# Performance work log

Hardware: AMD Instinct MI355X
Metric: run time of the kernel (lower is better)

Reference implementation:

```python
import jax, jax.numpy as jnp
import numpy as np

B, IN, T, E, S, K, W, HD = 4096, 512, 10, 16, 2, 4, 1024, 64


def setup_inputs() -> dict:
    key = jax.random.key(0)
    ks = jax.random.split(key, 12)
    he = lambda k, shp, fan: jax.random.normal(k, shp, jnp.float32) * (2.0 / fan) ** 0.5
    x = jax.random.normal(ks[0], (B, IN + T), jnp.float32)
    return {
        'x': x,
        'gk': he(ks[1], (T, E), T),
        'rk0': he(ks[2], (E, IN, W), IN),
        'rb0': jax.random.normal(ks[3], (E, W), jnp.float32) * 0.01,
        'rk1': he(ks[4], (E, W, W), W),
        'rb1': jax.random.normal(ks[5], (E, W), jnp.float32) * 0.01,
        'sk0': he(ks[6], (S, IN, W), IN),
        'sb0': jax.random.normal(ks[7], (S, W), jnp.float32) * 0.01,
        'sk1': he(ks[8], (S, W, W), W),
        'sb1': jax.random.normal(ks[9], (S, W), jnp.float32) * 0.01,
        'hk': he(ks[10], (T, W, HD), W),
        'hb': jax.random.normal(ks[11], (T, HD), jnp.float32) * 0.01,
    }


def reference(x, gk, rk0, rb0, rk1, rb1, sk0, sb0, sk1, sb1, hk, hb):
    task_idx = x[:, -T:]            # (B, T) task one-hot / features
    feat = x[:, :-T]                # (B, IN)

    # --- top-k routing on task features ---
    gating_logits = task_idx @ gk                       # (B, E)
    topk_idx = jnp.argsort(-gating_logits, axis=-1)[:, :K]  # (B, K)
    topk_logits = jnp.take_along_axis(gating_logits, topk_idx, axis=-1)
    topk_weights = jax.nn.softmax(topk_logits, axis=-1)     # (B, K)

    # --- routed experts: run every expert chain densely, gather at the end ---
    # h: (B, E, d); each expert's independent MLP chain over the same input.
    h = jnp.broadcast_to(feat[:, None, :], (B, E, IN))
    h = jax.nn.relu(jnp.einsum('bei,eij->bej', h, rk0) + rb0[None])  # (B, E, W)
    h = jax.nn.relu(jnp.einsum('bei,eij->bej', h, rk1) + rb1[None])  # (B, E, W)
    h_sel = jnp.take_along_axis(h, topk_idx[:, :, None], axis=1)     # (B, K, W)
    routed = jnp.einsum('bkw,bk->bw', h_sel, topk_weights)           # (B, W)

    # --- shared experts: all run, mean-combined ---
    hs = jnp.broadcast_to(feat[:, None, :], (B, S, IN))
    hs = jax.nn.relu(jnp.einsum('bsi,sij->bsj', hs, sk0) + sb0[None])
    hs = jax.nn.relu(jnp.einsum('bsi,sij->bsj', hs, sk1) + sb1[None])
    shared = hs.mean(axis=1)                                         # (B, W)

    features_out = jnp.tanh(routed + shared)                         # (B, W)

    # --- per-task heads, select by task id ---
    heads_out = jnp.einsum('bw,twd->btd', features_out, hk) + hb[None]  # (B, T, HD)
    task_indices = task_idx.argmax(axis=-1)                             # (B,)
    out = jnp.take_along_axis(heads_out, task_indices[:, None, None], axis=1)[:, 0]
    return out
```

## Files before the change

kernel.cpp:

```cpp
#include <hip/hip_runtime.h>

typedef unsigned short u16;
typedef __attribute__((ext_vector_type(8))) short bf16x8;
typedef __attribute__((ext_vector_type(4))) float f32x4;

constexpr int B_ = 4096, IN_ = 512, T_ = 10, E_ = 16, S_ = 2, K_ = 4, W_ = 1024, HD_ = 64;
constexpr int XROW = IN_ + T_;
constexpr int NPAIR = B_ * (K_ + S_);
constexpr int MTU = 208;
constexpr int GEMM_GRID = MTU * 8;
constexpr int GB_ = 16;
constexpr int CB_GRID = 1034;


#define GLL16(g, l) __builtin_amdgcn_global_load_lds( \
    (const __attribute__((address_space(1))) void*)(g), \
    (__attribute__((address_space(3))) void*)(l), 16, 0, 0)

__device__ __forceinline__ u16 f2bf(float x) {
    unsigned u = __float_as_uint(x);
    return (u16)((u + 0x7fffu + ((u >> 16) & 1u)) >> 16);
}
__device__ __forceinline__ float bf2f(u16 b) { return __uint_as_float(((unsigned)b) << 16); }

__global__ __launch_bounds__(256) void featconv(const float* __restrict__ x, u16* __restrict__ featb) {
    int i = blockIdx.x * 256 + threadIdx.x;
    int b = i >> 8;
    int c2 = (i & 255) * 2;
    float2 v = *(const float2*)(x + (size_t)b * XROW + c2);
    ushort2 o;
    o.x = f2bf(v.x);
    o.y = f2bf(v.y);
    *(ushort2*)(featb + (size_t)b * IN_ + c2) = o;
}

__global__ __launch_bounds__(256) void gate_kernel(const float* __restrict__ x, const float* __restrict__ gk,
                                                   int* __restrict__ top4p, float* __restrict__ w6,
                                                   int* __restrict__ task_id, int* __restrict__ tpp,
                                                   int* __restrict__ bct_e, int* __restrict__ bct_t) {
    __shared__ float sgk[T_ * E_];
    __shared__ int hist[E_];
    __shared__ int thist[T_];
    int blk = blockIdx.x, tid = threadIdx.x;
    int b = blk * 256 + tid;
    if (tid < T_ * E_) sgk[tid] = gk[tid];
    if (tid < E_) hist[tid] = 0;
    if (tid < T_) thist[tid] = 0;
    __syncthreads();
    float tv[T_];
#pragma unroll
    for (int i = 0; i < T_; ++i) tv[i] = x[(size_t)b * XROW + IN_ + i];
    float lg[E_];
#pragma unroll
    for (int e = 0; e < E_; ++e) {
        float s = 0.f;
#pragma unroll
        for (int i = 0; i < T_; ++i) s += tv[i] * sgk[i * E_ + e];
        lg[e] = s;
    }
    int idx[K_]; float val[K_];
#pragma unroll
    for (int k = 0; k < K_; ++k) {
        int bi = 0; float bv = -1e30f;
#pragma unroll
        for (int e = 0; e < E_; ++e)
            if (lg[e] > bv) { bv = lg[e]; bi = e; }
        idx[k] = bi; val[k] = bv; lg[bi] = -1e30f;
    }
    float m = val[0];
    float ex[K_]; float s = 0.f;
#pragma unroll
    for (int k = 0; k < K_; ++k) { ex[k] = expf(val[k] - m); s += ex[k]; }
    float inv = 1.f / s;
#pragma unroll
    for (int k = 0; k < K_; ++k) {
        int lp = atomicAdd(&hist[idx[k]], 1);
        top4p[b * K_ + k] = idx[k] | (lp << 8);
        w6[b * 6 + k] = ex[k] * inv;
    }
    w6[b * 6 + 4] = 0.5f;
    w6[b * 6 + 5] = 0.5f;
    int ti = 0; float tb = tv[0];
#pragma unroll
    for (int i = 1; i < T_; ++i)
        if (tv[i] > tb) { tb = tv[i]; ti = i; }
    task_id[b] = ti;
    tpp[b] = atomicAdd(&thist[ti], 1);
    __syncthreads();
    if (tid < E_) bct_e[blk * E_ + tid] = hist[tid];
    if (tid < T_) bct_t[blk * T_ + tid] = thist[tid];
}

__global__ void build_tables(const int* __restrict__ bct_e, const int* __restrict__ bct_t,
                             int* __restrict__ meta, int* __restrict__ blockbase,
                             int* __restrict__ tblockbase) {
    if (threadIdx.x != 0) return;
    int counts[E_];
    for (int e = 0; e < E_; ++e) {
        int s = 0;
        for (int blk = 0; blk < GB_; ++blk) s += bct_e[blk * E_ + e];
        counts[e] = s;
        meta[e] = s;
    }
    int a = 0;
    for (int e = 0; e < E_; ++e) { meta[16 + e] = a; a += counts[e]; }
    for (int e = 0; e < E_; ++e) {
        int run = meta[16 + e];
        for (int blk = 0; blk < GB_; ++blk) { blockbase[blk * E_ + e] = run; run += bct_e[blk * E_ + e]; }
    }
    int t = 0;
    for (int g = 0; g < 18; ++g) { meta[48 + g] = t; int c = (g < 16) ? counts[g] : B_; t += (c + 127) >> 7; }
    meta[66] = t;
    int tcnt[T_];
    for (int i = 0; i < T_; ++i) {
        int s = 0;
        for (int blk = 0; blk < GB_; ++blk) s += bct_t[blk * T_ + i];
        tcnt[i] = s;
        meta[91 + i] = s;
    }
    int pr = 0, br = 0;
    for (int i = 0; i < T_; ++i) {
        meta[70 + i] = pr;
        meta[80 + i] = br;
        pr += ((tcnt[i] + 3) >> 2) << 2;
        br += (tcnt[i] + 3) >> 2;
    }
    meta[90] = br;
    for (int i = 0; i < T_; ++i) {
        int run = meta[70 + i];
        for (int blk = 0; blk < GB_; ++blk) { tblockbase[blk * T_ + i] = run; run += bct_t[blk * T_ + i]; }
    }
}

__global__ __launch_bounds__(256) void scatter_kernel(const int* __restrict__ top4p,
                                                      const int* __restrict__ blockbase,
                                                      const int* __restrict__ task_id, const int* __restrict__ tpp,
                                                      const int* __restrict__ tblockbase,
                                                      int* __restrict__ pair_sample, int* __restrict__ pair_dst,
                                                      int* __restrict__ torder) {
    int blk = blockIdx.x, tid = threadIdx.x;
    int b = blk * 256 + tid;
#pragma unroll
    for (int k = 0; k < K_; ++k) {
        int v = top4p[b * K_ + k];
        int e = v & 0xFF, lp = v >> 8;
        int p = blockbase[blk * E_ + e] + lp;
        pair_sample[p] = b;
        pair_dst[p] = b * 6 + k;
    }
    pair_sample[B_ * K_ + b] = b;       pair_dst[B_ * K_ + b] = b * 6 + 4;
    pair_sample[B_ * K_ + B_ + b] = b;  pair_dst[B_ * K_ + B_ + b] = b * 6 + 5;
    torder[tblockbase[blk * T_ + task_id[b]] + tpp[b]] = b;
}

__global__ __launch_bounds__(256) void convbf16(const float* __restrict__ in, u16* __restrict__ out) {
    int i = blockIdx.x * 256 + threadIdx.x;
    float4 v = ((const float4*)in)[i];
    ushort4 o;
    o.x = f2bf(v.x); o.y = f2bf(v.y); o.z = f2bf(v.z); o.w = f2bf(v.w);
    ((ushort4*)out)[i] = o;
}

__global__ __launch_bounds__(256) void transconv2(const float* __restrict__ srcA, const float* __restrict__ srcB,
                                                  int splitZ, u16* __restrict__ out, int K, int N) {
    __shared__ float tile[32][33];
    int z = blockIdx.z;
    const float* src = (z < splitZ) ? (srcA + (size_t)z * K * N) : (srcB + (size_t)(z - splitZ) * K * N);
    int k0 = blockIdx.y * 32, n0 = blockIdx.x * 32;
    int tid = threadIdx.x;
    int r = tid >> 3, c4 = (tid & 7) * 4;
    float4 v = *(const float4*)(src + (size_t)(k0 + r) * N + n0 + c4);
    tile[r][c4 + 0] = v.x; tile[r][c4 + 1] = v.y; tile[r][c4 + 2] = v.z; tile[r][c4 + 3] = v.w;
    __syncthreads();
    ushort4 ov;
    ov.x = f2bf(tile[c4 + 0][r]);
    ov.y = f2bf(tile[c4 + 1][r]);
    ov.z = f2bf(tile[c4 + 2][r]);
    ov.w = f2bf(tile[c4 + 3][r]);
    *(ushort4*)(out + (size_t)z * N * K + (size_t)(n0 + r) * K + k0 + c4) = ov;
}

template <int K, int LAYER>
__global__ __launch_bounds__(256, 2) void gemm3(const u16* __restrict__ Asrc, const u16* __restrict__ wT,
                                                const float* __restrict__ rbias, const float* __restrict__ sbias,
                                                const int* __restrict__ pair_sample, const int* __restrict__ pair_dst,
                                                const int* __restrict__ meta, u16* __restrict__ outp) {
    __shared__ char lds[65536];
    const int* tpre = meta + 48;
    const int nwg = tpre[18] * 8;
    int p = blockIdx.x;
    if (p >= nwg) return;
    int q = nwg >> 3, r8 = nwg & 7;
    int xcd = p & 7, iofs = p >> 3;
    int lid = (xcd < r8 ? xcd * (q + 1) : r8 * (q + 1) + (xcd - r8) * q) + iofs;
    int mtu = lid >> 3, nt = lid & 7;
    int e = 0;
    while (mtu >= tpre[e + 1]) ++e;
    int mt = mtu - tpre[e];
    int off, cnt;
    if (e < E_) { off = meta[16 + e]; cnt = meta[e]; }
    else        { off = B_ * K_ + (e - E_) * B_; cnt = B_; }

    const int tid = threadIdx.x;
    const int srow = tid >> 3, sc = tid & 7;
    const u16* wTe = wT + (size_t)e * W_ * K;
    const u16* ab[4];
    const u16* bb[4];
#pragma unroll
    for (int r = 0; r < 4; ++r) {
        int row = r * 32 + srow;
        int swz = (sc ^ (row & 7)) * 8;
        int gm = mt * 128 + row;
        if (gm >= cnt) gm = cnt - 1;
        int arow = (LAYER == 1) ? pair_sample[off + gm] : (off + gm);
        ab[r] = Asrc + (size_t)arow * K + swz;
        bb[r] = wTe + (size_t)(nt * 128 + row) * K + swz;
    }

    auto STAGE = [&](int kt, int buf) {
        char* base = lds + buf * 32768;
#pragma unroll
        for (int r = 0; r < 4; ++r) GLL16(ab[r] + kt * 64, base + r * 4096 + tid * 16);
#pragma unroll
        for (int r = 0; r < 4; ++r) GLL16(bb[r] + kt * 64, base + 16384 + r * 4096 + tid * 16);
    };

    f32x4 acc[4][4];
#pragma unroll
    for (int i = 0; i < 4; ++i)
#pragma unroll
        for (int j = 0; j < 4; ++j) acc[i][j] = (f32x4){0.f, 0.f, 0.f, 0.f};

    const int lane = tid & 63, wid = tid >> 6;
    const int wr = wid >> 1, wc = wid & 1;
    const int fr = lane & 15;
    const int fkb = (lane >> 4) * 16;

    constexpr int NKT = K / 64;
    STAGE(0, 0);
    for (int kt = 0; kt < NKT; ++kt) {
        int cur = kt & 1;
        if (kt + 1 < NKT) {
            STAGE(kt + 1, cur ^ 1);
            asm volatile("s_waitcnt vmcnt(8)" ::: "memory");
        } else {
            asm volatile("s_waitcnt vmcnt(0)" ::: "memory");
        }
        __builtin_amdgcn_s_barrier();
        asm volatile("" ::: "memory");
        char* A = lds + cur * 32768;
        char* Bv = A + 16384;
#pragma unroll
        for (int kk = 0; kk < 2; ++kk) {
            bf16x8 af[4], bf[4];
#pragma unroll
            for (int i = 0; i < 4; ++i) {
                int arow = wr * 64 + i * 16 + fr;
                af[i] = *(const bf16x8*)(A + arow * 128 + ((kk * 64 + fkb) ^ ((arow & 7) << 4)));
                int brow = wc * 64 + i * 16 + fr;
                bf[i] = *(const bf16x8*)(Bv + brow * 128 + ((kk * 64 + fkb) ^ ((brow & 7) << 4)));
            }
            __builtin_amdgcn_s_setprio(1);
#pragma unroll
            for (int i = 0; i < 4; ++i)
#pragma unroll
                for (int j = 0; j < 4; ++j)
                    acc[i][j] = __builtin_amdgcn_mfma_f32_16x16x32_bf16(af[i], bf[j], acc[i][j], 0, 0, 0);
            __builtin_amdgcn_s_setprio(0);
        }
        asm volatile("" ::: "memory");
        __builtin_amdgcn_s_barrier();
    }

    __syncthreads();
    const float* bias = (e < E_) ? (rbias + (size_t)e * W_) : (sbias + (size_t)(e - E_) * W_);
#pragma unroll
    for (int i = 0; i < 4; ++i) {
#pragma unroll
        for (int reg = 0; reg < 4; ++reg) {
            int r = wr * 64 + i * 16 + (lane >> 4) * 4 + reg;
#pragma unroll
            for (int j = 0; j < 4; ++j) {
                int c = wc * 64 + j * 16 + fr;
                float v = acc[i][j][reg] + bias[nt * 128 + c];
                *(u16*)(lds + r * 272 + c * 2) = f2bf(fmaxf(v, 0.f));
            }
        }
    }
    __syncthreads();
#pragma unroll
    for (int rr = 0; rr < 8; ++rr) {
        int flat = rr * 4096 + tid * 16;
        int r = flat >> 8;
        int co = flat & 255;
        int m = mt * 128 + r;
        if (m < cnt) {
            int outrow = (LAYER == 1) ? (off + m) : pair_dst[off + m];
            bf16x8 v = *(const bf16x8*)(lds + r * 272 + co);
            *(bf16x8*)(outp + (size_t)outrow * W_ + nt * 128 + (co >> 1)) = v;
        }
    }
}

__global__ __launch_bounds__(256) void combine4(const u16* __restrict__ h2, const float* __restrict__ w6,
                                                const int* __restrict__ torder, const int* __restrict__ meta,
                                                const u16* __restrict__ hkb, const float* __restrict__ hb,
                                                float* __restrict__ out) {
    __shared__ float f[4][W_];
    __shared__ float partials[4][4][64];
    const int* bp = meta + 80;
    int blk = blockIdx.x;
    if (blk >= bp[T_]) return;
    int t = 0;
    while (blk >= bp[t + 1]) ++t;
    int slot0 = meta[70 + t] + (blk - bp[t]) * 4;
    int vend  = meta[70 + t] + meta[91 + t];
    int tid = threadIdx.x;
    int s0 = torder[slot0];
    int smp[4];
#pragma unroll
    for (int i = 0; i < 4; ++i) {
        int v = torder[slot0 + i];
        smp[i] = (slot0 + i < vend) ? v : s0;
    }
#pragma unroll
    for (int s = 0; s < 4; ++s) {
        int b = smp[s];
        float wsl[6];
#pragma unroll
        for (int q = 0; q < 6; ++q) wsl[q] = w6[b * 6 + q];
        float sum[4] = {0.f, 0.f, 0.f, 0.f};
#pragma unroll
        for (int q = 0; q < 6; ++q) {
            ushort4 v = *(const ushort4*)(h2 + (size_t)(b * 6 + q) * W_ + tid * 4);
            sum[0] += wsl[q] * bf2f(v.x);
            sum[1] += wsl[q] * bf2f(v.y);
            sum[2] += wsl[q] * bf2f(v.z);
            sum[3] += wsl[q] * bf2f(v.w);
        }
#pragma unroll
        for (int i = 0; i < 4; ++i) f[s][tid * 4 + i] = tanhf(sum[i]);
    }
    __syncthreads();
    int d = tid & 63, g = tid >> 6;
    const u16* hp = hkb + (size_t)t * W_ * HD_ + d;
    float acc[4] = {0.f, 0.f, 0.f, 0.f};
#pragma unroll 4
    for (int w = g; w < W_; w += 4) {
        float hv = bf2f(hp[(size_t)w * HD_]);
#pragma unroll
        for (int s = 0; s < 4; ++s) acc[s] += f[s][w] * hv;
    }
#pragma unroll
    for (int s = 0; s < 4; ++s) partials[g][s][d] = acc[s];
    __syncthreads();
    int ss = tid >> 6, dd = tid & 63;
    float r = partials[0][ss][dd] + partials[1][ss][dd] + partials[2][ss][dd] + partials[3][ss][dd]
            + hb[t * HD_ + dd];
    out[(size_t)smp[ss] * HD_ + dd] = r;
}

extern "C" void kernel_launch(void* const* d_in, const int* in_sizes, int n_in,
                              void* d_out, int out_size, void* d_ws, size_t ws_size,
                              hipStream_t stream) {
    const float* x   = (const float*)d_in[0];
    const float* gk  = (const float*)d_in[1];
    const float* rk0 = (const float*)d_in[2];
    const float* rb0 = (const float*)d_in[3];
    const float* rk1 = (const float*)d_in[4];
    const float* rb1 = (const float*)d_in[5];
    const float* sk0 = (const float*)d_in[6];
    const float* sb0 = (const float*)d_in[7];
    const float* sk1 = (const float*)d_in[8];
    const float* sb1 = (const float*)d_in[9];
    const float* hk  = (const float*)d_in[10];
    const float* hb  = (const float*)d_in[11];
    float* out = (float*)d_out;
    (void)in_sizes; (void)n_in; (void)out_size; (void)ws_size;

    char* ws = (char*)d_ws;
    size_t o = 0;
    auto alloc = [&](size_t bytes) { char* p = ws + o; o += (bytes + 255) & ~(size_t)255; return p; };
    int* meta        = (int*)alloc(512);
    int* bct_e       = (int*)alloc((size_t)GB_ * E_ * 4);
    int* bct_t       = (int*)alloc((size_t)GB_ * T_ * 4);
    int* blockbase   = (int*)alloc((size_t)GB_ * E_ * 4);
    int* tblockbase  = (int*)alloc((size_t)GB_ * T_ * 4);
    int* top4p       = (int*)alloc((size_t)B_ * K_ * 4);
    float* w6        = (float*)alloc((size_t)B_ * 6 * 4);
    int* task_id     = (int*)alloc((size_t)B_ * 4);
    int* tpp         = (int*)alloc((size_t)B_ * 4);
    int* pair_sample = (int*)alloc((size_t)NPAIR * 4);
    int* pair_dst    = (int*)alloc((size_t)NPAIR * 4);
    int* torder      = (int*)alloc((size_t)(B_ + 64) * 4);
    u16* featb       = (u16*)alloc((size_t)B_ * IN_ * 2);
    u16* w0T         = (u16*)alloc((size_t)(E_ + S_) * W_ * IN_ * 2);
    u16* w1T         = (u16*)alloc((size_t)(E_ + S_) * W_ * W_ * 2);
    u16* hkb         = (u16*)alloc((size_t)T_ * W_ * HD_ * 2);
    u16* h1          = (u16*)alloc((size_t)NPAIR * W_ * 2);
    u16* h2          = (u16*)alloc((size_t)NPAIR * W_ * 2);

    featconv<<<B_, 256, 0, stream>>>(x, featb);
    gate_kernel<<<GB_, 256, 0, stream>>>(x, gk, top4p, w6, task_id, tpp, bct_e, bct_t);
    build_tables<<<1, 64, 0, stream>>>(bct_e, bct_t, meta, blockbase, tblockbase);
    scatter_kernel<<<GB_, 256, 0, stream>>>(top4p, blockbase, task_id, tpp, tblockbase,
                                            pair_sample, pair_dst, torder);
    transconv2<<<dim3(W_ / 32, IN_ / 32, E_ + S_), 256, 0, stream>>>(rk0, sk0, E_, w0T, IN_, W_);
    transconv2<<<dim3(W_ / 32, W_ / 32, E_ + S_), 256, 0, stream>>>(rk1, sk1, E_, w1T, W_, W_);
    convbf16<<<(T_ * W_ * HD_) / 1024, 256, 0, stream>>>(hk, hkb);
    gemm3<IN_, 1><<<GEMM_GRID, 256, 0, stream>>>(featb, w0T, rb0, sb0, pair_sample, pair_dst, meta, h1);
    gemm3<W_, 2><<<GEMM_GRID, 256, 0, stream>>>(h1, w1T, rb1, sb1, pair_sample, pair_dst, meta, h2);
    combine4<<<CB_GRID, 256, 0, stream>>>(h2, w6, torder, meta, hkb, hb, out);
}
```

Baseline: 204.5 us.

## Fuse both expert MLP layers into one kernel keeping h1 in LDS

Replaces the two separate grouped GEMM launches with one fused kernel. Each 512-thread workgroup handles 64 rows of one expert, computes layer 1 over the full width into a 128KB LDS buffer, then runs layer 2 from LDS. This removes the h1 round trip through global memory and one launch. In exchange, the operand tiles are no longer staged: A and B fragments are read directly from global memory with no double buffering, so each workgroup streams the full expert weights. The 128KB LDS limits occupancy to one workgroup per CU, and the 32-tile accumulator arrays raise register pressure.

```diff
diff --git a/kernel.cpp b/kernel.cpp
--- a/kernel.cpp
+++ b/kernel.cpp
@@ -7,15 +7,10 @@
 constexpr int B_ = 4096, IN_ = 512, T_ = 10, E_ = 16, S_ = 2, K_ = 4, W_ = 1024, HD_ = 64;
 constexpr int XROW = IN_ + T_;
 constexpr int NPAIR = B_ * (K_ + S_);
-constexpr int MTU = 208;
-constexpr int GEMM_GRID = MTU * 8;
+constexpr int FUSED_GRID = 400;
 constexpr int GB_ = 16;
 constexpr int CB_GRID = 1034;
 
-
-#define GLL16(g, l) __builtin_amdgcn_global_load_lds( \
-    (const __attribute__((address_space(1))) void*)(g), \
-    (__attribute__((address_space(3))) void*)(l), 16, 0, 0)
 
 __device__ __forceinline__ u16 f2bf(float x) {
     unsigned u = __float_as_uint(x);
@@ -109,7 +104,7 @@
         for (int blk = 0; blk < GB_; ++blk) { blockbase[blk * E_ + e] = run; run += bct_e[blk * E_ + e]; }
     }
     int t = 0;
-    for (int g = 0; g < 18; ++g) { meta[48 + g] = t; int c = (g < 16) ? counts[g] : B_; t += (c + 127) >> 7; }
+    for (int g = 0; g < 18; ++g) { meta[48 + g] = t; int c = (g < 16) ? counts[g] : B_; t += (c + 63) >> 6; }
     meta[66] = t;
     int tcnt[T_];
     for (int i = 0; i < T_; ++i) {
@@ -180,20 +175,21 @@
     *(ushort4*)(out + (size_t)z * N * K + (size_t)(n0 + r) * K + k0 + c4) = ov;
 }
 
-template <int K, int LAYER>
-__global__ __launch_bounds__(256, 2) void gemm3(const u16* __restrict__ Asrc, const u16* __restrict__ wT,
-                                                const float* __restrict__ rbias, const float* __restrict__ sbias,
-                                                const int* __restrict__ pair_sample, const int* __restrict__ pair_dst,
-                                                const int* __restrict__ meta, u16* __restrict__ outp) {
-    __shared__ char lds[65536];
+__global__ __launch_bounds__(512, 2) void moe_fused(const u16* __restrict__ featb, const u16* __restrict__ w0T,
+                                                    const u16* __restrict__ w1T,
+                                                    const float* __restrict__ rb0, const float* __restrict__ sb0,
+                                                    const float* __restrict__ rb1, const float* __restrict__ sb1,
+                                                    const int* __restrict__ pair_sample,
+                                                    const int* __restrict__ pair_dst,
+                                                    const int* __restrict__ meta, u16* __restrict__ h2) {
+    __shared__ char h1[64 * 2048];
     const int* tpre = meta + 48;
-    const int nwg = tpre[18] * 8;
+    const int nwg = tpre[18];
     int p = blockIdx.x;
     if (p >= nwg) return;
     int q = nwg >> 3, r8 = nwg & 7;
     int xcd = p & 7, iofs = p >> 3;
-    int lid = (xcd < r8 ? xcd * (q + 1) : r8 * (q + 1) + (xcd - r8) * q) + iofs;
-    int mtu = lid >> 3, nt = lid & 7;
+    int mtu = (xcd < r8 ? xcd * (q + 1) : r8 * (q + 1) + (xcd - r8) * q) + iofs;
     int e = 0;
     while (mtu >= tpre[e + 1]) ++e;
     int mt = mtu - tpre[e];
@@ -202,102 +198,99 @@
     else        { off = B_ * K_ + (e - E_) * B_; cnt = B_; }
 
     const int tid = threadIdx.x;
-    const int srow = tid >> 3, sc = tid & 7;
-    const u16* wTe = wT + (size_t)e * W_ * K;
-    const u16* ab[4];
-    const u16* bb[4];
-#pragma unroll
-    for (int r = 0; r < 4; ++r) {
-        int row = r * 32 + srow;
-        int swz = (sc ^ (row & 7)) * 8;
-        int gm = mt * 128 + row;
+    const int lane = tid & 63, w = tid >> 6;
+    const int fr = lane & 15, kc = lane >> 4;
+
+    int psmp[4], pdst[4];
+#pragma unroll
+    for (int mi = 0; mi < 4; ++mi) {
+        int gm = mt * 64 + mi * 16 + fr;
         if (gm >= cnt) gm = cnt - 1;
-        int arow = (LAYER == 1) ? pair_sample[off + gm] : (off + gm);
-        ab[r] = Asrc + (size_t)arow * K + swz;
-        bb[r] = wTe + (size_t)(nt * 128 + row) * K + swz;
-    }
-
-    auto STAGE = [&](int kt, int buf) {
-        char* base = lds + buf * 32768;
-#pragma unroll
-        for (int r = 0; r < 4; ++r) GLL16(ab[r] + kt * 64, base + r * 4096 + tid * 16);
-#pragma unroll
-        for (int r = 0; r < 4; ++r) GLL16(bb[r] + kt * 64, base + 16384 + r * 4096 + tid * 16);
-    };
-
-    f32x4 acc[4][4];
-#pragma unroll
-    for (int i = 0; i < 4; ++i)
-#pragma unroll
-        for (int j = 0; j < 4; ++j) acc[i][j] = (f32x4){0.f, 0.f, 0.f, 0.f};
-
-    const int lane = tid & 63, wid = tid >> 6;
-    const int wr = wid >> 1, wc = wid & 1;
-    const int fr = lane & 15;
-    const int fkb = (lane >> 4) * 16;
-
-    constexpr int NKT = K / 64;
-    STAGE(0, 0);
-    for (int kt = 0; kt < NKT; ++kt) {
-        int cur = kt & 1;
-        if (kt + 1 < NKT) {
-            STAGE(kt + 1, cur ^ 1);
-            asm volatile("s_waitcnt vmcnt(8)" ::: "memory");
-        } else {
-            asm volatile("s_waitcnt vmcnt(0)" ::: "memory");
+        psmp[mi] = pair_sample[off + gm];
+        pdst[mi] = pair_dst[off + gm];
+    }
+    const u16* w0e = w0T + (size_t)e * W_ * IN_;
+    const u16* w1e = w1T + (size_t)e * W_ * W_;
+    const float* b1 = (e < E_) ? rb0 + (size_t)e * W_ : sb0 + (size_t)(e - E_) * W_;
+    const float* b2 = (e < E_) ? rb1 + (size_t)e * W_ : sb1 + (size_t)(e - E_) * W_;
+
+    f32x4 acc[8][4];
+#pragma unroll
+    for (int nj = 0; nj < 8; ++nj)
+#pragma unroll
+        for (int mi = 0; mi < 4; ++mi) acc[nj][mi] = (f32x4){0.f, 0.f, 0.f, 0.f};
+
+    for (int kt = 0; kt < IN_ / 64; ++kt) {
+#pragma unroll
+        for (int kk = 0; kk < 2; ++kk) {
+            const int ko = kt * 64 + kk * 32 + kc * 8;
+            bf16x8 va[8], vb[4];
+#pragma unroll
+            for (int nj = 0; nj < 8; ++nj)
+                va[nj] = *(const bf16x8*)(w0e + (size_t)(w * 128 + nj * 16 + fr) * IN_ + ko);
+#pragma unroll
+            for (int mi = 0; mi < 4; ++mi)
+                vb[mi] = *(const bf16x8*)(featb + (size_t)psmp[mi] * IN_ + ko);
+#pragma unroll
+            for (int nj = 0; nj < 8; ++nj)
+#pragma unroll
+                for (int mi = 0; mi < 4; ++mi)
+                    acc[nj][mi] = __builtin_amdgcn_mfma_f32_16x16x32_bf16(va[nj], vb[mi], acc[nj][mi], 0, 0, 0);
         }
-        __builtin_amdgcn_s_barrier();
-        asm volatile("" ::: "memory");
-        char* A = lds + cur * 32768;
-        char* Bv = A + 16384;
+    }
+#pragma unroll
+    for (int nj = 0; nj < 8; ++nj) {
+        int n0 = w * 128 + nj * 16 + kc * 4;
+        float4 bb = *(const float4*)(b1 + n0);
+#pragma unroll
+        for (int mi = 0; mi < 4; ++mi) {
+            int r = mi * 16 + fr;
+            u16 o[4];
+            o[0] = f2bf(fmaxf(acc[nj][mi][0] + bb.x, 0.f));
+            o[1] = f2bf(fmaxf(acc[nj][mi][1] + bb.y, 0.f));
+            o[2] = f2bf(fmaxf(acc[nj][mi][2] + bb.z, 0.f));
+            o[3] = f2bf(fmaxf(acc[nj][mi][3] + bb.w, 0.f));
+            *(uint2*)(h1 + r * 2048 + ((n0 * 2) ^ ((r & 7) << 4))) = *(const uint2*)o;
+        }
+    }
+    __syncthreads();
+
+#pragma unroll
+    for (int nj = 0; nj < 8; ++nj)
+#pragma unroll
+        for (int mi = 0; mi < 4; ++mi) acc[nj][mi] = (f32x4){0.f, 0.f, 0.f, 0.f};
+    for (int kt = 0; kt < W_ / 64; ++kt) {
 #pragma unroll
         for (int kk = 0; kk < 2; ++kk) {
-            bf16x8 af[4], bf[4];
-#pragma unroll
-            for (int i = 0; i < 4; ++i) {
-                int arow = wr * 64 + i * 16 + fr;
-                af[i] = *(const bf16x8*)(A + arow * 128 + ((kk * 64 + fkb) ^ ((arow & 7) << 4)));
-                int brow = wc * 64 + i * 16 + fr;
-                bf[i] = *(const bf16x8*)(Bv + brow * 128 + ((kk * 64 + fkb) ^ ((brow & 7) << 4)));
+            const int ko = kt * 64 + kk * 32 + kc * 8;
+            bf16x8 va[8], vb[4];
+#pragma unroll
+            for (int nj = 0; nj < 8; ++nj)
+                va[nj] = *(const bf16x8*)(w1e + (size_t)(w * 128 + nj * 16 + fr) * W_ + ko);
+#pragma unroll
+            for (int mi = 0; mi < 4; ++mi) {
+                int r = mi * 16 + fr;
+                vb[mi] = *(const bf16x8*)(h1 + r * 2048 + ((ko * 2) ^ ((r & 7) << 4)));
             }
-            __builtin_amdgcn_s_setprio(1);
-#pragma unroll
-            for (int i = 0; i < 4; ++i)
-#pragma unroll
-                for (int j = 0; j < 4; ++j)
-                    acc[i][j] = __builtin_amdgcn_mfma_f32_16x16x32_bf16(af[i], bf[j], acc[i][j], 0, 0, 0);
-            __builtin_amdgcn_s_setprio(0);
+#pragma unroll
+            for (int nj = 0; nj < 8; ++nj)
+#pragma unroll
+                for (int mi = 0; mi < 4; ++mi)
+                    acc[nj][mi] = __builtin_amdgcn_mfma_f32_16x16x32_bf16(va[nj], vb[mi], acc[nj][mi], 0, 0, 0);
         }
-        asm volatile("" ::: "memory");
-        __builtin_amdgcn_s_barrier();
-    }
-
-    __syncthreads();
-    const float* bias = (e < E_) ? (rbias + (size_t)e * W_) : (sbias + (size_t)(e - E_) * W_);
-#pragma unroll
-    for (int i = 0; i < 4; ++i) {
-#pragma unroll
-        for (int reg = 0; reg < 4; ++reg) {
-            int r = wr * 64 + i * 16 + (lane >> 4) * 4 + reg;
-#pragma unroll
-            for (int j = 0; j < 4; ++j) {
-                int c = wc * 64 + j * 16 + fr;
-                float v = acc[i][j][reg] + bias[nt * 128 + c];
-                *(u16*)(lds + r * 272 + c * 2) = f2bf(fmaxf(v, 0.f));
-            }
-        }
-    }
-    __syncthreads();
-#pragma unroll
-    for (int rr = 0; rr < 8; ++rr) {
-        int flat = rr * 4096 + tid * 16;
-        int r = flat >> 8;
-        int co = flat & 255;
-        int m = mt * 128 + r;
-        if (m < cnt) {
-            int outrow = (LAYER == 1) ? (off + m) : pair_dst[off + m];
-            bf16x8 v = *(const bf16x8*)(lds + r * 272 + co);
-            *(bf16x8*)(outp + (size_t)outrow * W_ + nt * 128 + (co >> 1)) = v;
+    }
+#pragma unroll
+    for (int nj = 0; nj < 8; ++nj) {
+        int n0 = w * 128 + nj * 16 + kc * 4;
+        float4 bb = *(const float4*)(b2 + n0);
+#pragma unroll
+        for (int mi = 0; mi < 4; ++mi) {
+            u16 o[4];
+            o[0] = f2bf(fmaxf(acc[nj][mi][0] + bb.x, 0.f));
+            o[1] = f2bf(fmaxf(acc[nj][mi][1] + bb.y, 0.f));
+            o[2] = f2bf(fmaxf(acc[nj][mi][2] + bb.z, 0.f));
+            o[3] = f2bf(fmaxf(acc[nj][mi][3] + bb.w, 0.f));
+            *(uint2*)(h2 + (size_t)pdst[mi] * W_ + n0) = *(const uint2*)o;
         }
     }
 }
@@ -328,15 +321,15 @@
         int b = smp[s];
         float wsl[6];
 #pragma unroll
-        for (int q = 0; q < 6; ++q) wsl[q] = w6[b * 6 + q];
+        for (int qq = 0; qq < 6; ++qq) wsl[qq] = w6[b * 6 + qq];
         float sum[4] = {0.f, 0.f, 0.f, 0.f};
 #pragma unroll
-        for (int q = 0; q < 6; ++q) {
-            ushort4 v = *(const ushort4*)(h2 + (size_t)(b * 6 + q) * W_ + tid * 4);
-            sum[0] += wsl[q] * bf2f(v.x);
-            sum[1] += wsl[q] * bf2f(v.y);
-            sum[2] += wsl[q] * bf2f(v.z);
-            sum[3] += wsl[q] * bf2f(v.w);
+        for (int qq = 0; qq < 6; ++qq) {
+            ushort4 v = *(const ushort4*)(h2 + (size_t)(b * 6 + qq) * W_ + tid * 4);
+            sum[0] += wsl[qq] * bf2f(v.x);
+            sum[1] += wsl[qq] * bf2f(v.y);
+            sum[2] += wsl[qq] * bf2f(v.z);
+            sum[3] += wsl[qq] * bf2f(v.w);
         }
 #pragma unroll
         for (int i = 0; i < 4; ++i) f[s][tid * 4 + i] = tanhf(sum[i]);
@@ -397,7 +390,6 @@
     u16* w0T         = (u16*)alloc((size_t)(E_ + S_) * W_ * IN_ * 2);
     u16* w1T         = (u16*)alloc((size_t)(E_ + S_) * W_ * W_ * 2);
     u16* hkb         = (u16*)alloc((size_t)T_ * W_ * HD_ * 2);
-    u16* h1          = (u16*)alloc((size_t)NPAIR * W_ * 2);
     u16* h2          = (u16*)alloc((size_t)NPAIR * W_ * 2);
 
     featconv<<<B_, 256, 0, stream>>>(x, featb);
@@ -408,7 +400,7 @@
     transconv2<<<dim3(W_ / 32, IN_ / 32, E_ + S_), 256, 0, stream>>>(rk0, sk0, E_, w0T, IN_, W_);
     transconv2<<<dim3(W_ / 32, W_ / 32, E_ + S_), 256, 0, stream>>>(rk1, sk1, E_, w1T, W_, W_);
     convbf16<<<(T_ * W_ * HD_) / 1024, 256, 0, stream>>>(hk, hkb);
-    gemm3<IN_, 1><<<GEMM_GRID, 256, 0, stream>>>(featb, w0T, rb0, sb0, pair_sample, pair_dst, meta, h1);
-    gemm3<W_, 2><<<GEMM_GRID, 256, 0, stream>>>(h1, w1T, rb1, sb1, pair_sample, pair_dst, meta, h2);
+    moe_fused<<<FUSED_GRID, 512, 0, stream>>>(featb, w0T, w1T, rb0, sb0, rb1, sb1,
+                                              pair_sample, pair_dst, meta, h2);
     combine4<<<CB_GRID, 256, 0, stream>>>(h2, w6, torder, meta, hkb, hb, out);
 }
```

Result: slower. 314.4 us (+53.8%).

## Drop LDS double buffering in grouped GEMM to fit four blocks per CU

Applied to the files above, without the earlier changes.

The expert GEMM kernel now uses a single 32KB LDS buffer instead of a double-buffered 64KB one, raising launch bounds from 2 to 4 blocks per CU. Each k-step loads its tile, syncs, computes and syncs again, with the s_setprio hints removed. The intent is to hide memory latency through more resident blocks rather than in-block prefetch. The epilogue staging changes from a padded 272-byte row stride to an XOR-swizzled 256-byte stride so it fits the smaller buffer. The tighter register budget from the higher launch bound may cause spills, and the in-block load/compute overlap is lost.

```diff
diff --git a/kernel.cpp b/kernel.cpp
--- a/kernel.cpp
+++ b/kernel.cpp
@@ -181,11 +181,11 @@
 }
 
 template <int K, int LAYER>
-__global__ __launch_bounds__(256, 2) void gemm3(const u16* __restrict__ Asrc, const u16* __restrict__ wT,
+__global__ __launch_bounds__(256, 4) void gemm4(const u16* __restrict__ Asrc, const u16* __restrict__ wT,
                                                 const float* __restrict__ rbias, const float* __restrict__ sbias,
                                                 const int* __restrict__ pair_sample, const int* __restrict__ pair_dst,
                                                 const int* __restrict__ meta, u16* __restrict__ outp) {
-    __shared__ char lds[65536];
+    __shared__ char lds[32768];
     const int* tpre = meta + 48;
     const int nwg = tpre[18] * 8;
     int p = blockIdx.x;
@@ -217,14 +217,6 @@
         bb[r] = wTe + (size_t)(nt * 128 + row) * K + swz;
     }
 
-    auto STAGE = [&](int kt, int buf) {
-        char* base = lds + buf * 32768;
-#pragma unroll
-        for (int r = 0; r < 4; ++r) GLL16(ab[r] + kt * 64, base + r * 4096 + tid * 16);
-#pragma unroll
-        for (int r = 0; r < 4; ++r) GLL16(bb[r] + kt * 64, base + 16384 + r * 4096 + tid * 16);
-    };
-
     f32x4 acc[4][4];
 #pragma unroll
     for (int i = 0; i < 4; ++i)
@@ -237,42 +229,31 @@
     const int fkb = (lane >> 4) * 16;
 
     constexpr int NKT = K / 64;
-    STAGE(0, 0);
     for (int kt = 0; kt < NKT; ++kt) {
-        int cur = kt & 1;
-        if (kt + 1 < NKT) {
-            STAGE(kt + 1, cur ^ 1);
-            asm volatile("s_waitcnt vmcnt(8)" ::: "memory");
-        } else {
-            asm volatile("s_waitcnt vmcnt(0)" ::: "memory");
-        }
-        __builtin_amdgcn_s_barrier();
-        asm volatile("" ::: "memory");
-        char* A = lds + cur * 32768;
-        char* Bv = A + 16384;
+#pragma unroll
+        for (int r = 0; r < 4; ++r) GLL16(ab[r] + kt * 64, lds + r * 4096 + tid * 16);
+#pragma unroll
+        for (int r = 0; r < 4; ++r) GLL16(bb[r] + kt * 64, lds + 16384 + r * 4096 + tid * 16);
+        __syncthreads();
 #pragma unroll
         for (int kk = 0; kk < 2; ++kk) {
             bf16x8 af[4], bf[4];
 #pragma unroll
             for (int i = 0; i < 4; ++i) {
                 int arow = wr * 64 + i * 16 + fr;
-                af[i] = *(const bf16x8*)(A + arow * 128 + ((kk * 64 + fkb) ^ ((arow & 7) << 4)));
+                af[i] = *(const bf16x8*)(lds + arow * 128 + ((kk * 64 + fkb) ^ ((arow & 7) << 4)));
                 int brow = wc * 64 + i * 16 + fr;
-                bf[i] = *(const bf16x8*)(Bv + brow * 128 + ((kk * 64 + fkb) ^ ((brow & 7) << 4)));
+                bf[i] = *(const bf16x8*)(lds + 16384 + brow * 128 + ((kk * 64 + fkb) ^ ((brow & 7) << 4)));
             }
-            __builtin_amdgcn_s_setprio(1);
 #pragma unroll
             for (int i = 0; i < 4; ++i)
 #pragma unroll
                 for (int j = 0; j < 4; ++j)
                     acc[i][j] = __builtin_amdgcn_mfma_f32_16x16x32_bf16(af[i], bf[j], acc[i][j], 0, 0, 0);
-            __builtin_amdgcn_s_setprio(0);
         }
-        asm volatile("" ::: "memory");
-        __builtin_amdgcn_s_barrier();
-    }
-
-    __syncthreads();
+        __syncthreads();
+    }
+
     const float* bias = (e < E_) ? (rbias + (size_t)e * W_) : (sbias + (size_t)(e - E_) * W_);
 #pragma unroll
     for (int i = 0; i < 4; ++i) {
@@ -283,7 +264,7 @@
             for (int j = 0; j < 4; ++j) {
                 int c = wc * 64 + j * 16 + fr;
                 float v = acc[i][j][reg] + bias[nt * 128 + c];
-                *(u16*)(lds + r * 272 + c * 2) = f2bf(fmaxf(v, 0.f));
+                *(u16*)(lds + r * 256 + ((c * 2) ^ ((r & 7) << 4))) = f2bf(fmaxf(v, 0.f));
             }
         }
     }
@@ -296,7 +277,7 @@
         int m = mt * 128 + r;
         if (m < cnt) {
             int outrow = (LAYER == 1) ? (off + m) : pair_dst[off + m];
-            bf16x8 v = *(const bf16x8*)(lds + r * 272 + co);
+            bf16x8 v = *(const bf16x8*)(lds + r * 256 + (co ^ ((r & 7) << 4)));
             *(bf16x8*)(outp + (size_t)outrow * W_ + nt * 128 + (co >> 1)) = v;
         }
     }
@@ -328,15 +309,15 @@
         int b = smp[s];
         float wsl[6];
 #pragma unroll
-        for (int q = 0; q < 6; ++q) wsl[q] = w6[b * 6 + q];
+        for (int qq = 0; qq < 6; ++qq) wsl[qq] = w6[b * 6 + qq];
         float sum[4] = {0.f, 0.f, 0.f, 0.f};
 #pragma unroll
-        for (int q = 0; q < 6; ++q) {
-            ushort4 v = *(const ushort4*)(h2 + (size_t)(b * 6 + q) * W_ + tid * 4);
-            sum[0] += wsl[q] * bf2f(v.x);
-            sum[1] += wsl[q] * bf2f(v.y);
-            sum[2] += wsl[q] * bf2f(v.z);
-            sum[3] += wsl[q] * bf2f(v.w);
+        for (int qq = 0; qq < 6; ++qq) {
+            ushort4 v = *(const ushort4*)(h2 + (size_t)(b * 6 + qq) * W_ + tid * 4);
+            sum[0] += wsl[qq] * bf2f(v.x);
+            sum[1] += wsl[qq] * bf2f(v.y);
+            sum[2] += wsl[qq] * bf2f(v.z);
+            sum[3] += wsl[qq] * bf2f(v.w);
         }
 #pragma unroll
         for (int i = 0; i < 4; ++i) f[s][tid * 4 + i] = tanhf(sum[i]);
@@ -408,7 +389,7 @@
     transconv2<<<dim3(W_ / 32, IN_ / 32, E_ + S_), 256, 0, stream>>>(rk0, sk0, E_, w0T, IN_, W_);
     transconv2<<<dim3(W_ / 32, W_ / 32, E_ + S_), 256, 0, stream>>>(rk1, sk1, E_, w1T, W_, W_);
     convbf16<<<(T_ * W_ * HD_) / 1024, 256, 0, stream>>>(hk, hkb);
-    gemm3<IN_, 1><<<GEMM_GRID, 256, 0, stream>>>(featb, w0T, rb0, sb0, pair_sample, pair_dst, meta, h1);
-    gemm3<W_, 2><<<GEMM_GRID, 256, 0, stream>>>(h1, w1T, rb1, sb1, pair_sample, pair_dst, meta, h2);
+    gemm4<IN_, 1><<<GEMM_GRID, 256, 0, stream>>>(featb, w0T, rb0, sb0, pair_sample, pair_dst, meta, h1);
+    gemm4<W_, 2><<<GEMM_GRID, 256, 0, stream>>>(h1, w1T, rb1, sb1, pair_sample, pair_dst, meta, h2);
     combine4<<<CB_GRID, 256, 0, stream>>>(h2, w6, torder, meta, hkb, hb, out);
 }
```

Result: no change. 204.1 us (-0.2%).
